# Kernel tuning notes

Hardware: AMD Instinct MI355X
Metric: run time of the kernel (lower is better)

The kernel has to match this reference:

```python
import jax, jax.numpy as jnp
import numpy as np

B, S, H = 4, 4096, 2880
E, K = 32, 4


def setup_inputs() -> dict:
    key = jax.random.key(0)
    k1, k2 = jax.random.split(key)
    hidden_states = jax.random.normal(k1, (B, S, H), dtype=jnp.float32)
    # router weight, scaled like a typical init (std ~ 1/sqrt(H))
    weight = jax.random.normal(k2, (E, H), dtype=jnp.float32) / np.sqrt(H)
    bias = jnp.zeros((E,), dtype=jnp.float32)
    return {"hidden_states": hidden_states, "weight": weight, "bias": bias}


def reference(hidden_states, weight, bias):
    b, s, h = hidden_states.shape
    x = hidden_states.reshape(-1, h)                     # [T, H]
    logits = jnp.einsum('th,eh->te', x, weight) + bias   # [T, E]
    # select top-k logits (sorted descending), then softmax over the subset
    topk_logits, topk_idx = jax.lax.top_k(logits, K)     # [T, K]
    topk_weight = jax.nn.softmax(topk_logits.astype(jnp.float32), axis=-1)
    return topk_idx, topk_weight
```

## Files before the change

### kernel.cpp

```cpp
#include <hip/hip_runtime.h>
#include <math.h>

#define H_DIM 2880
#define E_NUM 32
#define TOPK 4
#define TT 16
#define KW 96
#define NSTG 30
#define GRP 776
#define XBS 1552
#define WB0 3104
#define WBS 3104
#define SMSZ 9312
#define REDR 36
#define LGTO 2304

#define GLD16(gp, lp)                                                  \
    __builtin_amdgcn_global_load_lds(                                  \
        (const __attribute__((address_space(1))) void*)(gp),           \
        (__attribute__((address_space(3))) void*)(lp), 16, 0, 0)

__global__ __launch_bounds__(256, 4) void gate_fused(
    const float* __restrict__ x, const float* __restrict__ w,
    const float* __restrict__ bias, float* __restrict__ out, int T) {
    __shared__ float sm[SMSZ];
    const int tid = threadIdx.x;
    const int lane = tid & 63;
    const int wq = __builtin_amdgcn_readfirstlane(tid >> 6);
    const int tt = lane & 3;
    const int et = (lane >> 2) & 3;
    const int ksl = lane >> 4;
    const int t0 = blockIdx.x * TT;

    const float* gw[3]; int lw[3];
    const float* gx[3]; int lx[3];
#pragma unroll
    for (int i = 0; i < 3; ++i) {
        const int d = i * 256 + lane * 4;
        const int r = d / KW, kk = d % KW;
        gw[i] = w + (size_t)(wq * 8 + r) * H_DIM + kk;
        lw[i] = WB0 + wq * GRP + d;
        const int xr = (wq & 1) * 8 + r;
        gx[i] = x + (size_t)(t0 + xr) * H_DIM + kk;
        lx[i] = (wq & 1) * GRP + d;
    }

    float acc[32];
#pragma unroll
    for (int i = 0; i < 32; ++i) acc[i] = 0.f;

#pragma unroll
    for (int i = 0; i < 3; ++i) GLD16(gw[i], &sm[lw[i]]);
    if (wq < 2) {
#pragma unroll
        for (int i = 0; i < 3; ++i) GLD16(gx[i], &sm[lx[i]]);
    }

    const int ks = wq * 4 + ksl;
    const int koA = ks * 4;
    const int koB = 64 + ks * 2;
    const int xln = (tt >> 1) * GRP + (tt & 1) * (4 * KW);
    const int wln = et * GRP;

    for (int s = 0; s < NSTG; ++s) {
        asm volatile("s_waitcnt vmcnt(0)" ::: "memory");
        __builtin_amdgcn_s_barrier();
        asm volatile("" ::: "memory");

        if (s + 1 < NSTG) {
            const size_t go = (size_t)(s + 1) * KW;
            const int b = (s + 1) & 1;
#pragma unroll
            for (int i = 0; i < 3; ++i) GLD16(gw[i] + go, &sm[lw[i] + b * WBS]);
            if (wq < 2) {
#pragma unroll
                for (int i = 0; i < 3; ++i) GLD16(gx[i] + go, &sm[lx[i] + b * XBS]);
            }
        }

        const int p = s & 1;
        const float* xb = &sm[p * XBS + xln];
        const float* wb = &sm[WB0 + p * WBS + wln];

        float4 xa[4]; float2 xc[4];
#pragma unroll
        for (int i = 0; i < 4; ++i) xa[i] = *(const float4*)(xb + i * KW + koA);
#pragma unroll
        for (int i = 0; i < 4; ++i) xc[i] = *(const float2*)(xb + i * KW + koB);
#pragma unroll
        for (int j = 0; j < 8; ++j) {
            const float4 wv = *(const float4*)(wb + j * KW + koA);
            const float2 wc = *(const float2*)(wb + j * KW + koB);
#pragma unroll
            for (int i = 0; i < 4; ++i)
                acc[i * 8 + j] += xa[i].x * wv.x + xa[i].y * wv.y +
                                  xa[i].z * wv.z + xa[i].w * wv.w +
                                  xc[i].x * wc.x + xc[i].y * wc.y;
        }
    }

    __syncthreads();

#pragma unroll
    for (int d = 0; d < 32; ++d) {
        acc[d] += __shfl_xor(acc[d], 16, 64);
        acc[d] += __shfl_xor(acc[d], 32, 64);
    }

    if (ksl == 0) {
#pragma unroll
        for (int i = 0; i < 4; ++i) {
            float* rp = &sm[wq * (TT * REDR) + (tt * 4 + i) * REDR + et * 8];
            *(float4*)(rp + 0) = make_float4(acc[i * 8 + 0], acc[i * 8 + 1],
                                             acc[i * 8 + 2], acc[i * 8 + 3]);
            *(float4*)(rp + 4) = make_float4(acc[i * 8 + 4], acc[i * 8 + 5],
                                             acc[i * 8 + 6], acc[i * 8 + 7]);
        }
    }
    __syncthreads();

    if (tid < 128) {
        const int tok = tid >> 3, e4 = (tid & 7) * 4;
        float4 sg = *(const float4*)(bias + e4);
#pragma unroll
        for (int q = 0; q < 4; ++q) {
            float4 v = *(const float4*)&sm[q * (TT * REDR) + tok * REDR + e4];
            sg.x += v.x; sg.y += v.y; sg.z += v.z; sg.w += v.w;
        }
        *(float4*)&sm[LGTO + tok * REDR + e4] = sg;
    }
    __syncthreads();

    if (tid < TT) {
        const int t = t0 + tid;
        float logit[E_NUM];
#pragma unroll
        for (int j = 0; j < 8; ++j) {
            float4 v = *(const float4*)&sm[LGTO + tid * REDR + j * 4];
            logit[j * 4] = v.x; logit[j * 4 + 1] = v.y;
            logit[j * 4 + 2] = v.z; logit[j * 4 + 3] = v.w;
        }

        int idx[TOPK];
        float val[TOPK];
#pragma unroll
        for (int k = 0; k < TOPK; ++k) {
            float best = -INFINITY;
            int bi = 0;
#pragma unroll
            for (int e = 0; e < E_NUM; ++e) {
                bool taken = false;
                for (int p2 = 0; p2 < k; ++p2) taken = taken || (idx[p2] == e);
                float v = logit[e];
                if (!taken && v > best) { best = v; bi = e; }
            }
            idx[k] = bi;
            val[k] = best;
        }
        float ex[TOPK], ssum = 0.f;
#pragma unroll
        for (int k = 0; k < TOPK; ++k) { ex[k] = expf(val[k] - val[0]); ssum += ex[k]; }
        const float inv = 1.f / ssum;

        *(float4*)(out + (size_t)t * 4) =
            make_float4((float)idx[0], (float)idx[1], (float)idx[2], (float)idx[3]);
        *(float4*)(out + (size_t)T * 4 + (size_t)t * 4) =
            make_float4(ex[0] * inv, ex[1] * inv, ex[2] * inv, ex[3] * inv);
    }
}

extern "C" void kernel_launch(void* const* d_in, const int* in_sizes, int n_in,
                              void* d_out, int out_size, void* d_ws, size_t ws_size,
                              hipStream_t stream) {
    const float* x    = (const float*)d_in[0];
    const float* w    = (const float*)d_in[1];
    const float* bias = (const float*)d_in[2];
    float* out = (float*)d_out;

    const int T = in_sizes[0] / H_DIM;

    gate_fused<<<dim3(T / TT), 256, 0, stream>>>(x, w, bias, out, T);
}
```

Baseline: 275.5 us.

## Replace LDS double-buffered staging with direct register-prefetched global loads

The kernel no longer stages x and weight tiles through LDS with async global-to-LDS loads and per-stage barriers. Each thread now loads its x and weight float4 slices straight into registers with software double-buffering, and each wave owns 8 experts. Partial sums are reduced with wave shuffles before writing logits to a small LDS array. This removes barrier and LDS traffic, at the cost of more redundant global/L2 reads of weights and x across waves and higher register pressure.

```diff
diff --git a/kernel.cpp b/kernel.cpp
--- a/kernel.cpp
+++ b/kernel.cpp
@@ -5,129 +5,92 @@
 #define E_NUM 32
 #define TOPK 4
 #define TT 16
-#define KW 96
-#define NSTG 30
-#define GRP 776
-#define XBS 1552
-#define WB0 3104
-#define WBS 3104
-#define SMSZ 9312
-#define REDR 36
-#define LGTO 2304
-
-#define GLD16(gp, lp)                                                  \
-    __builtin_amdgcn_global_load_lds(                                  \
-        (const __attribute__((address_space(1))) void*)(gp),           \
-        (__attribute__((address_space(3))) void*)(lp), 16, 0, 0)
+#define KW 64
+#define NSTG 45
+#define LGR 36
 
 __global__ __launch_bounds__(256, 4) void gate_fused(
     const float* __restrict__ x, const float* __restrict__ w,
     const float* __restrict__ bias, float* __restrict__ out, int T) {
-    __shared__ float sm[SMSZ];
+    __shared__ float lg[TT * LGR];
     const int tid = threadIdx.x;
     const int lane = tid & 63;
     const int wq = __builtin_amdgcn_readfirstlane(tid >> 6);
     const int tt = lane & 3;
-    const int et = (lane >> 2) & 3;
-    const int ksl = lane >> 4;
+    const int ks = lane >> 2;
     const int t0 = blockIdx.x * TT;
+    const int ks4 = ks * 4;
 
-    const float* gw[3]; int lw[3];
-    const float* gx[3]; int lx[3];
+    const float* xr[4];
 #pragma unroll
-    for (int i = 0; i < 3; ++i) {
-        const int d = i * 256 + lane * 4;
-        const int r = d / KW, kk = d % KW;
-        gw[i] = w + (size_t)(wq * 8 + r) * H_DIM + kk;
-        lw[i] = WB0 + wq * GRP + d;
-        const int xr = (wq & 1) * 8 + r;
-        gx[i] = x + (size_t)(t0 + xr) * H_DIM + kk;
-        lx[i] = (wq & 1) * GRP + d;
+    for (int i = 0; i < 4; ++i)
+        xr[i] = x + (size_t)(t0 + tt * 4 + i) * H_DIM + ks4;
+    const float* wrow[8];
+#pragma unroll
+    for (int j = 0; j < 8; ++j)
+        wrow[j] = w + (size_t)(wq * 8 + j) * H_DIM;
+
+    float acc[4][8];
+#pragma unroll
+    for (int i = 0; i < 4; ++i)
+#pragma unroll
+        for (int j = 0; j < 8; ++j) acc[i][j] = 0.f;
+
+    float4 xA[4], xB[4], wc[8];
+    int soff = ks4;
+#pragma unroll
+    for (int i = 0; i < 4; ++i) { xA[i] = *(const float4*)xr[i]; xr[i] += KW; }
+#pragma unroll
+    for (int j = 0; j < 8; ++j) wc[j] = *(const float4*)(wrow[j] + soff);
+
+#define STAGE_R(XC, XN)                                                     \
+    do {                                                                    \
+        _Pragma("unroll")                                                   \
+        for (int i = 0; i < 4; ++i) {                                       \
+            XN[i] = *(const float4*)xr[i];                                  \
+            xr[i] += KW;                                                    \
+        }                                                                   \
+        soff += KW;                                                         \
+        _Pragma("unroll")                                                   \
+        for (int j = 0; j < 8; ++j) {                                       \
+            _Pragma("unroll")                                               \
+            for (int i = 0; i < 4; ++i)                                     \
+                acc[i][j] += XC[i].x * wc[j].x + XC[i].y * wc[j].y +        \
+                             XC[i].z * wc[j].z + XC[i].w * wc[j].w;         \
+            wc[j] = *(const float4*)(wrow[j] + soff);                       \
+        }                                                                   \
+    } while (0)
+
+    for (int it = 0; it < (NSTG - 1) / 2; ++it) {
+        STAGE_R(xA, xB);
+        STAGE_R(xB, xA);
     }
-
-    float acc[32];
 #pragma unroll
-    for (int i = 0; i < 32; ++i) acc[i] = 0.f;
+    for (int j = 0; j < 8; ++j)
+#pragma unroll
+        for (int i = 0; i < 4; ++i)
+            acc[i][j] += xA[i].x * wc[j].x + xA[i].y * wc[j].y +
+                         xA[i].z * wc[j].z + xA[i].w * wc[j].w;
 
 #pragma unroll
-    for (int i = 0; i < 3; ++i) GLD16(gw[i], &sm[lw[i]]);
-    if (wq < 2) {
+    for (int i = 0; i < 4; ++i)
 #pragma unroll
-        for (int i = 0; i < 3; ++i) GLD16(gx[i], &sm[lx[i]]);
-    }
-
-    const int ks = wq * 4 + ksl;
-    const int koA = ks * 4;
-    const int koB = 64 + ks * 2;
-    const int xln = (tt >> 1) * GRP + (tt & 1) * (4 * KW);
-    const int wln = et * GRP;
-
-    for (int s = 0; s < NSTG; ++s) {
-        asm volatile("s_waitcnt vmcnt(0)" ::: "memory");
-        __builtin_amdgcn_s_barrier();
-        asm volatile("" ::: "memory");
-
-        if (s + 1 < NSTG) {
-            const size_t go = (size_t)(s + 1) * KW;
-            const int b = (s + 1) & 1;
-#pragma unroll
-            for (int i = 0; i < 3; ++i) GLD16(gw[i] + go, &sm[lw[i] + b * WBS]);
-            if (wq < 2) {
-#pragma unroll
-                for (int i = 0; i < 3; ++i) GLD16(gx[i] + go, &sm[lx[i] + b * XBS]);
-            }
+        for (int j = 0; j < 8; ++j) {
+            float v = acc[i][j];
+            v += __shfl_xor(v, 4, 64);
+            v += __shfl_xor(v, 8, 64);
+            v += __shfl_xor(v, 16, 64);
+            v += __shfl_xor(v, 32, 64);
+            acc[i][j] = v;
         }
 
-        const int p = s & 1;
-        const float* xb = &sm[p * XBS + xln];
-        const float* wb = &sm[WB0 + p * WBS + wln];
-
-        float4 xa[4]; float2 xc[4];
+    if (ks == 0) {
 #pragma unroll
-        for (int i = 0; i < 4; ++i) xa[i] = *(const float4*)(xb + i * KW + koA);
+        for (int i = 0; i < 4; ++i)
 #pragma unroll
-        for (int i = 0; i < 4; ++i) xc[i] = *(const float2*)(xb + i * KW + koB);
-#pragma unroll
-        for (int j = 0; j < 8; ++j) {
-            const float4 wv = *(const float4*)(wb + j * KW + koA);
-            const float2 wc = *(const float2*)(wb + j * KW + koB);
-#pragma unroll
-            for (int i = 0; i < 4; ++i)
-                acc[i * 8 + j] += xa[i].x * wv.x + xa[i].y * wv.y +
-                                  xa[i].z * wv.z + xa[i].w * wv.w +
-                                  xc[i].x * wc.x + xc[i].y * wc.y;
-        }
-    }
-
-    __syncthreads();
-
-#pragma unroll
-    for (int d = 0; d < 32; ++d) {
-        acc[d] += __shfl_xor(acc[d], 16, 64);
-        acc[d] += __shfl_xor(acc[d], 32, 64);
-    }
-
-    if (ksl == 0) {
-#pragma unroll
-        for (int i = 0; i < 4; ++i) {
-            float* rp = &sm[wq * (TT * REDR) + (tt * 4 + i) * REDR + et * 8];
-            *(float4*)(rp + 0) = make_float4(acc[i * 8 + 0], acc[i * 8 + 1],
-                                             acc[i * 8 + 2], acc[i * 8 + 3]);
-            *(float4*)(rp + 4) = make_float4(acc[i * 8 + 4], acc[i * 8 + 5],
-                                             acc[i * 8 + 6], acc[i * 8 + 7]);
-        }
-    }
-    __syncthreads();
-
-    if (tid < 128) {
-        const int tok = tid >> 3, e4 = (tid & 7) * 4;
-        float4 sg = *(const float4*)(bias + e4);
-#pragma unroll
-        for (int q = 0; q < 4; ++q) {
-            float4 v = *(const float4*)&sm[q * (TT * REDR) + tok * REDR + e4];
-            sg.x += v.x; sg.y += v.y; sg.z += v.z; sg.w += v.w;
-        }
-        *(float4*)&sm[LGTO + tok * REDR + e4] = sg;
+            for (int j = 0; j < 8; ++j)
+                lg[(tt * 4 + i) * LGR + wq * 8 + j] =
+                    acc[i][j] + bias[wq * 8 + j];
     }
     __syncthreads();
 
@@ -135,10 +98,10 @@
         const int t = t0 + tid;
         float logit[E_NUM];
 #pragma unroll
-        for (int j = 0; j < 8; ++j) {
-            float4 v = *(const float4*)&sm[LGTO + tid * REDR + j * 4];
-            logit[j * 4] = v.x; logit[j * 4 + 1] = v.y;
-            logit[j * 4 + 2] = v.z; logit[j * 4 + 3] = v.w;
+        for (int j2 = 0; j2 < 8; ++j2) {
+            float4 v = *(const float4*)&lg[tid * LGR + j2 * 4];
+            logit[j2 * 4] = v.x; logit[j2 * 4 + 1] = v.y;
+            logit[j2 * 4 + 2] = v.z; logit[j2 * 4 + 3] = v.w;
         }
 
         int idx[TOPK];
```

Result: slower. 615.5 us (+123.5%).

## Load activations directly to registers, enlarge token tile, stage only weights in LDS

Applied to the files above, without the earlier changes.

The token tile grows from 16 to 32 tokens and the K chunk shrinks to 64 columns over 45 stages. Activations now go straight from global memory into registers as float4 loads, prefetched one stage ahead, and only the router weights are double-buffered in LDS. Each thread accumulates 8 tokens by 8 experts. The aim is to halve how often the weight matrix is reread per token and to remove the LDS round-trip for the activations. The cost is more registers: occupancy is pinned to 2 waves per EU, and the per-thread global activation loads are strided rather than coalesced.

```diff
diff --git a/kernel.cpp b/kernel.cpp
--- a/kernel.cpp
+++ b/kernel.cpp
@@ -4,23 +4,22 @@
 #define H_DIM 2880
 #define E_NUM 32
 #define TOPK 4
-#define TT 16
-#define KW 96
-#define NSTG 30
-#define GRP 776
-#define XBS 1552
-#define WB0 3104
-#define WBS 3104
-#define SMSZ 9312
+#define TT 32
+#define KW 64
+#define NSTG 45
+#define WSTRIDE 512
+#define WBUF 2048
 #define REDR 36
-#define LGTO 2304
+#define LGTO 4608
+#define SMSZ 5760
 
 #define GLD16(gp, lp)                                                  \
     __builtin_amdgcn_global_load_lds(                                  \
         (const __attribute__((address_space(1))) void*)(gp),           \
         (__attribute__((address_space(3))) void*)(lp), 16, 0, 0)
 
-__global__ __launch_bounds__(256, 4) void gate_fused(
+__global__ __attribute__((amdgpu_flat_work_group_size(256, 256),
+                          amdgpu_waves_per_eu(2, 2))) void gate_fused(
     const float* __restrict__ x, const float* __restrict__ w,
     const float* __restrict__ bias, float* __restrict__ out, int T) {
     __shared__ float sm[SMSZ];
@@ -31,95 +30,105 @@
     const int et = (lane >> 2) & 3;
     const int ksl = lane >> 4;
     const int t0 = blockIdx.x * TT;
+    const int ksd = wq * 16 + ksl * 4;
 
-    const float* gw[3]; int lw[3];
-    const float* gx[3]; int lx[3];
-#pragma unroll
-    for (int i = 0; i < 3; ++i) {
-        const int d = i * 256 + lane * 4;
-        const int r = d / KW, kk = d % KW;
-        gw[i] = w + (size_t)(wq * 8 + r) * H_DIM + kk;
-        lw[i] = WB0 + wq * GRP + d;
-        const int xr = (wq & 1) * 8 + r;
-        gx[i] = x + (size_t)(t0 + xr) * H_DIM + kk;
-        lx[i] = (wq & 1) * GRP + d;
-    }
+    const int d0 = lane * 4, d1 = 256 + lane * 4;
+    const float* gw0 = w + (size_t)(wq * 8 + d0 / KW) * H_DIM + (d0 % KW);
+    const float* gw1 = w + (size_t)(wq * 8 + d1 / KW) * H_DIM + (d1 % KW);
+    const int lw0 = wq * WSTRIDE + d0;
+    const int lw1 = wq * WSTRIDE + d1;
 
-    float acc[32];
-#pragma unroll
-    for (int i = 0; i < 32; ++i) acc[i] = 0.f;
+    const float* xb = x + (size_t)t0 * H_DIM;
+    int xo0 = (tt * 8 + 0) * H_DIM + ksd, xo1 = (tt * 8 + 1) * H_DIM + ksd;
+    int xo2 = (tt * 8 + 2) * H_DIM + ksd, xo3 = (tt * 8 + 3) * H_DIM + ksd;
+    int xo4 = (tt * 8 + 4) * H_DIM + ksd, xo5 = (tt * 8 + 5) * H_DIM + ksd;
+    int xo6 = (tt * 8 + 6) * H_DIM + ksd, xo7 = (tt * 8 + 7) * H_DIM + ksd;
 
-#pragma unroll
-    for (int i = 0; i < 3; ++i) GLD16(gw[i], &sm[lw[i]]);
-    if (wq < 2) {
-#pragma unroll
-        for (int i = 0; i < 3; ++i) GLD16(gx[i], &sm[lx[i]]);
-    }
+    float4 a0l = make_float4(0.f, 0.f, 0.f, 0.f), a0h = a0l, a1l = a0l, a1h = a0l;
+    float4 a2l = a0l, a2h = a0l, a3l = a0l, a3h = a0l;
+    float4 a4l = a0l, a4h = a0l, a5l = a0l, a5h = a0l;
+    float4 a6l = a0l, a6h = a0l, a7l = a0l, a7h = a0l;
+    float4 xq0, xq1, xq2, xq3, xq4, xq5, xq6, xq7, wA, wB;
 
-    const int ks = wq * 4 + ksl;
-    const int koA = ks * 4;
-    const int koB = 64 + ks * 2;
-    const int xln = (tt >> 1) * GRP + (tt & 1) * (4 * KW);
-    const int wln = et * GRP;
+    GLD16(gw0, &sm[lw0]); GLD16(gw1, &sm[lw1]);
+    gw0 += KW; gw1 += KW;
+    xq0 = *(const float4*)(xb + xo0); xq1 = *(const float4*)(xb + xo1);
+    xq2 = *(const float4*)(xb + xo2); xq3 = *(const float4*)(xb + xo3);
+    xq4 = *(const float4*)(xb + xo4); xq5 = *(const float4*)(xb + xo5);
+    xq6 = *(const float4*)(xb + xo6); xq7 = *(const float4*)(xb + xo7);
 
+#define DOT(XQ, WQ) (XQ.x * WQ.x + XQ.y * WQ.y + XQ.z * WQ.z + XQ.w * WQ.w)
+#define FMAE(AL, AH, WQ)                                               \
+    do {                                                               \
+        AL.x += DOT(xq0, WQ); AL.y += DOT(xq1, WQ);                    \
+        AL.z += DOT(xq2, WQ); AL.w += DOT(xq3, WQ);                    \
+        AH.x += DOT(xq4, WQ); AH.y += DOT(xq5, WQ);                    \
+        AH.z += DOT(xq6, WQ); AH.w += DOT(xq7, WQ);                    \
+    } while (0)
+
+#pragma unroll 1
     for (int s = 0; s < NSTG; ++s) {
         asm volatile("s_waitcnt vmcnt(0)" ::: "memory");
         __builtin_amdgcn_s_barrier();
         asm volatile("" ::: "memory");
 
         if (s + 1 < NSTG) {
-            const size_t go = (size_t)(s + 1) * KW;
-            const int b = (s + 1) & 1;
-#pragma unroll
-            for (int i = 0; i < 3; ++i) GLD16(gw[i] + go, &sm[lw[i] + b * WBS]);
-            if (wq < 2) {
-#pragma unroll
-                for (int i = 0; i < 3; ++i) GLD16(gx[i] + go, &sm[lx[i] + b * XBS]);
-            }
+            const int pn = (s + 1) & 1;
+            GLD16(gw0, &sm[lw0 + pn * WBUF]);
+            GLD16(gw1, &sm[lw1 + pn * WBUF]);
+            gw0 += KW; gw1 += KW;
         }
 
-        const int p = s & 1;
-        const float* xb = &sm[p * XBS + xln];
-        const float* wb = &sm[WB0 + p * WBS + wln];
+        const float* wp = &sm[(s & 1) * WBUF + et * (8 * KW) + ksd];
+        wA = *(const float4*)(wp + 0 * KW);
+        wB = *(const float4*)(wp + 1 * KW); FMAE(a0l, a0h, wA);
+        wA = *(const float4*)(wp + 2 * KW); FMAE(a1l, a1h, wB);
+        wB = *(const float4*)(wp + 3 * KW); FMAE(a2l, a2h, wA);
+        wA = *(const float4*)(wp + 4 * KW); FMAE(a3l, a3h, wB);
+        wB = *(const float4*)(wp + 5 * KW); FMAE(a4l, a4h, wA);
+        wA = *(const float4*)(wp + 6 * KW); FMAE(a5l, a5h, wB);
+        wB = *(const float4*)(wp + 7 * KW); FMAE(a6l, a6h, wA);
+        FMAE(a7l, a7h, wB);
 
-        float4 xa[4]; float2 xc[4];
-#pragma unroll
-        for (int i = 0; i < 4; ++i) xa[i] = *(const float4*)(xb + i * KW + koA);
-#pragma unroll
-        for (int i = 0; i < 4; ++i) xc[i] = *(const float2*)(xb + i * KW + koB);
-#pragma unroll
-        for (int j = 0; j < 8; ++j) {
-            const float4 wv = *(const float4*)(wb + j * KW + koA);
-            const float2 wc = *(const float2*)(wb + j * KW + koB);
-#pragma unroll
-            for (int i = 0; i < 4; ++i)
-                acc[i * 8 + j] += xa[i].x * wv.x + xa[i].y * wv.y +
-                                  xa[i].z * wv.z + xa[i].w * wv.w +
-                                  xc[i].x * wc.x + xc[i].y * wc.y;
+        if (s + 1 < NSTG) {
+            xo0 += KW; xo1 += KW; xo2 += KW; xo3 += KW;
+            xo4 += KW; xo5 += KW; xo6 += KW; xo7 += KW;
+            xq0 = *(const float4*)(xb + xo0); xq1 = *(const float4*)(xb + xo1);
+            xq2 = *(const float4*)(xb + xo2); xq3 = *(const float4*)(xb + xo3);
+            xq4 = *(const float4*)(xb + xo4); xq5 = *(const float4*)(xb + xo5);
+            xq6 = *(const float4*)(xb + xo6); xq7 = *(const float4*)(xb + xo7);
         }
     }
 
     __syncthreads();
 
-#pragma unroll
-    for (int d = 0; d < 32; ++d) {
-        acc[d] += __shfl_xor(acc[d], 16, 64);
-        acc[d] += __shfl_xor(acc[d], 32, 64);
-    }
+#define FOLD4(V)                                        \
+    do {                                                \
+        V.x += __shfl_xor(V.x, 16, 64); V.x += __shfl_xor(V.x, 32, 64); \
+        V.y += __shfl_xor(V.y, 16, 64); V.y += __shfl_xor(V.y, 32, 64); \
+        V.z += __shfl_xor(V.z, 16, 64); V.z += __shfl_xor(V.z, 32, 64); \
+        V.w += __shfl_xor(V.w, 16, 64); V.w += __shfl_xor(V.w, 32, 64); \
+    } while (0)
+    FOLD4(a0l); FOLD4(a0h); FOLD4(a1l); FOLD4(a1h);
+    FOLD4(a2l); FOLD4(a2h); FOLD4(a3l); FOLD4(a3h);
+    FOLD4(a4l); FOLD4(a4h); FOLD4(a5l); FOLD4(a5h);
+    FOLD4(a6l); FOLD4(a6h); FOLD4(a7l); FOLD4(a7h);
 
     if (ksl == 0) {
-#pragma unroll
-        for (int i = 0; i < 4; ++i) {
-            float* rp = &sm[wq * (TT * REDR) + (tt * 4 + i) * REDR + et * 8];
-            *(float4*)(rp + 0) = make_float4(acc[i * 8 + 0], acc[i * 8 + 1],
-                                             acc[i * 8 + 2], acc[i * 8 + 3]);
-            *(float4*)(rp + 4) = make_float4(acc[i * 8 + 4], acc[i * 8 + 5],
-                                             acc[i * 8 + 6], acc[i * 8 + 7]);
-        }
+#define STROW(I, HF, CP)                                                     \
+    do {                                                                     \
+        float* rp = &sm[wq * (TT * REDR) + (tt * 8 + I) * REDR + et * 8];    \
+        *(float4*)(rp + 0) =                                                 \
+            make_float4(a0##HF.CP, a1##HF.CP, a2##HF.CP, a3##HF.CP);         \
+        *(float4*)(rp + 4) =                                                 \
+            make_float4(a4##HF.CP, a5##HF.CP, a6##HF.CP, a7##HF.CP);         \
+    } while (0)
+        STROW(0, l, x); STROW(1, l, y); STROW(2, l, z); STROW(3, l, w);
+        STROW(4, h, x); STROW(5, h, y); STROW(6, h, z); STROW(7, h, w);
     }
     __syncthreads();
 
-    if (tid < 128) {
+    {
         const int tok = tid >> 3, e4 = (tid & 7) * 4;
         float4 sg = *(const float4*)(bias + e4);
 #pragma unroll
```

Measured after the change: 317.2 us. +15.1%, slower.
